# Optimization experiments

Measured on AMD Instinct MI355X. Metric: run time of the kernel, lower is better.

The kernel has to match this reference:

```python
import jax, jax.numpy as jnp
import numpy as np

N, K, D = 32768, 8192, 64

def setup_inputs() -> dict:
    key = jax.random.key(0)
    kx, kc = jax.random.split(key)
    x = jax.random.normal(kx, (N, D), dtype=jnp.float32)
    codebook = jax.random.normal(kc, (K, D), dtype=jnp.float32)
    return {"x": x, "codebook": codebook}

def reference(x, codebook):
    # Faithful to: argmin(((codebook[None] - x[:, None])**2).sum(-1), -1)
    # Computed via the expanded squared distance to avoid the [N, K, D]
    # constant per row and does not affect argmin, but we include it so the
    # distance matrix matches the original math exactly.
    x_sq = jnp.sum(x * x, axis=-1, keepdims=True)          # [N, 1]
    c_sq = jnp.sum(codebook * codebook, axis=-1)           # [K]
    cross = jnp.einsum('nd,kd->nk', x, codebook)           # [N, K]
    dists = x_sq - 2.0 * cross + c_sq[None, :]             # [N, K]
    return jnp.argmin(dists, axis=-1)                      # [N] int32
```

## Files before the change

kernel.cpp:

```cpp
#include <hip/hip_runtime.h>
#include <math.h>


typedef __attribute__((ext_vector_type(8)))  _Float16 h8v;
typedef __attribute__((ext_vector_type(16))) float f16v;

constexpr int NROWS = 32768;
constexpr int KC    = 8192;
constexpr int DD    = 64;
constexpr int TPB   = 512;
constexpr int PTPB  = 256;
constexpr int BROWS = 128;
constexpr int BTILE = 128;
constexpr int NT    = KC / BTILE;
constexpr int TILE_HALFS = BTILE * DD * 2;
constexpr int BUF_HALFS  = TILE_HALFS + 256;

__device__ __forceinline__ void split2h(float v, _Float16& h1, _Float16& h2) {
  const float av = fabsf(v);
  _Float16 a = (_Float16)v;
  if (av < 6.1035156e-5f) a = (_Float16)0.f;
  h1 = a;
  h2 = (_Float16)((v - (float)a) * 4096.f);
}

__device__ __forceinline__ void gload_lds16(const void* g, void* l) {
  __builtin_amdgcn_global_load_lds(
      (const __attribute__((address_space(1))) void*)g,
      (__attribute__((address_space(3))) void*)l, 16, 0, 0);
}
__device__ __forceinline__ void gload_lds4(const void* g, void* l) {
  __builtin_amdgcn_global_load_lds(
      (const __attribute__((address_space(1))) void*)g,
      (__attribute__((address_space(3))) void*)l, 4, 0, 0);
}

__device__ __forceinline__ unsigned fkey(float f) {
  const unsigned u = __float_as_uint(f);
  return u ^ (((unsigned)((int)u >> 31)) | 0x80000000u);
}

__global__ void vq_pre_kernel(const float* __restrict__ cb,
                              _Float16* __restrict__ bSwz,
                              float* __restrict__ csq) {
  const int gidx = blockIdx.x * PTPB + threadIdx.x;
  const int code = gidx >> 2;
  const int kc4  = gidx & 3;
  const float* cp = cb + (size_t)code * DD + kc4 * 16;
  float v[16];
#pragma unroll
  for (int d = 0; d < 16; d += 4) {
    const float4 g = *(const float4*)(cp + d);
    v[d] = g.x; v[d + 1] = g.y; v[d + 2] = g.z; v[d + 3] = g.w;
  }
  float s = 0.f;
#pragma unroll
  for (int d = 0; d < 16; ++d) s = fmaf(v[d], v[d], s);
  s += __shfl_xor(s, 1, 64);
  s += __shfl_xor(s, 2, 64);
  if (kc4 == 0) csq[code] = s;
  _Float16 p1[16], p2[16];
#pragma unroll
  for (int d = 0; d < 16; ++d) split2h(v[d], p1[d], p2[d]);
  const int g = code >> 5, l = code & 31;
  _Float16* base = bSwz + (size_t)g * 4096;
#pragma unroll
  for (int p = 0; p < 2; ++p) {
    const _Float16* pl = p ? p2 : p1;
#pragma unroll
    for (int h = 0; h < 2; ++h) {
      h8v wv;
#pragma unroll
      for (int j = 0; j < 8; ++j) wv[j] = pl[h * 8 + j];
      *(h8v*)(base + (p * 4 + kc4) * 512 + (h * 32 + l) * 8) = wv;
    }
  }
}

__global__ __launch_bounds__(TPB, 2)
void vq_mfma_kernel(const float* __restrict__ x, const _Float16* __restrict__ bSwz,
                    const float* __restrict__ csq_g, int* __restrict__ out) {
  __shared__ alignas(16) _Float16 ldsBf[3 * BUF_HALFS];
  __shared__ alignas(16) unsigned long long ldsRed[BROWS][4];

  const int tid  = threadIdx.x;
  const int lane = tid & 63;
  const int w    = tid >> 6;
  const int cg   = w & 3;
  const int rh   = w >> 2;
  const int half = lane >> 5;
  const int col  = lane & 31;
  const int wcode = cg * 32 + col;
  const int blockRow = blockIdx.x * BROWS;

#pragma unroll
  for (int tt = 0; tt < 2; ++tt) {
    const _Float16* gs = bSwz + (size_t)tt * TILE_HALFS + w * 512 + lane * 8;
    _Float16* ld = ldsBf + tt * BUF_HALFS + w * 512;
#pragma unroll
    for (int seg = 0; seg < 4; ++seg)
      gload_lds16(gs + seg * 4096, ld + seg * 4096);
    if (w < 2)
      gload_lds4(csq_g + tt * BTILE + w * 64 + lane,
                 (float*)(ldsBf + tt * BUF_HALFS + TILE_HALFS) + w * 64);
  }

  _Float16* ldsA2 = ldsBf + 2 * BUF_HALFS;
  {
    const int row = tid >> 2, dseg = (tid & 3) * 16;
    const float* xp = x + (size_t)(blockRow + row) * DD + dseg;
    float v[16];
#pragma unroll
    for (int d = 0; d < 16; d += 4) {
      const float4 g = *(const float4*)(xp + d);
      v[d] = g.x; v[d + 1] = g.y; v[d + 2] = g.z; v[d + 3] = g.w;
    }
    _Float16 qa[16], qb[16];
#pragma unroll
    for (int e = 0; e < 16; ++e) split2h(v[e], qa[e], qb[e]);
#pragma unroll
    for (int h2 = 0; h2 < 2; ++h2) {
      h8v a, b;
#pragma unroll
      for (int j = 0; j < 8; ++j) { a[j] = qa[h2 * 8 + j]; b[j] = qb[h2 * 8 + j]; }
      const int slot = (tid & 3) * 2 + h2;
      *(h8v*)&ldsA2[((0 * BROWS + row) * 8 + (slot ^ (row & 7))) * 8] = a;
      *(h8v*)&ldsA2[((1 * BROWS + row) * 8 + (slot ^ (row & 7))) * 8] = b;
    }
  }
  asm volatile("s_waitcnt lgkmcnt(0)\n\ts_barrier" ::: "memory");

  h8v afr[2][2][4];
#pragma unroll
  for (int q = 0; q < 2; ++q)
#pragma unroll
    for (int p = 0; p < 2; ++p)
#pragma unroll
      for (int kc = 0; kc < 4; ++kc) {
        const int arow = rh * 64 + q * 32 + col;
        const int slot = kc * 2 + half;
        afr[q][p][kc] =
            *(const h8v*)&ldsA2[((p * BROWS + arow) * 8 + (slot ^ (arow & 7))) * 8];
      }
  asm volatile("s_waitcnt vmcnt(4) lgkmcnt(0)\n\ts_barrier" ::: "memory");

  float bestD[32];
  unsigned bestC[32];
#pragma unroll
  for (int i = 0; i < 32; ++i) { bestD[i] = INFINITY; bestC[i] = 0u; }

  const f16v Z = {0.f,0.f,0.f,0.f,0.f,0.f,0.f,0.f,0.f,0.f,0.f,0.f,0.f,0.f,0.f,0.f};

  int buf = 0, pf = 2;
  for (int t = 0; t < NT; ++t) {
    if (t < NT - 2) {
      const _Float16* gs = bSwz + (size_t)(t + 2) * TILE_HALFS + w * 512 + lane * 8;
      _Float16* ld = ldsBf + pf * BUF_HALFS + w * 512;
#pragma unroll
      for (int seg = 0; seg < 4; ++seg)
        gload_lds16(gs + seg * 4096, ld + seg * 4096);
      if (w < 2)
        gload_lds4(csq_g + (t + 2) * BTILE + w * 64 + lane,
                   (float*)(ldsBf + pf * BUF_HALFS + TILE_HALFS) + w * 64);
    }
    const _Float16* bp = ldsBf + buf * BUF_HALFS;
    const _Float16* rb = bp + cg * 4096 + lane * 8;
    h8v b0[4], b1[4];
#pragma unroll
    for (int kc = 0; kc < 4; ++kc) {
      b0[kc] = *(const h8v*)(rb + kc * 512);
      b1[kc] = *(const h8v*)(rb + (4 + kc) * 512);
    }
    const float cs = ((const float*)(bp + TILE_HALFS))[wcode];

    f16v A0 = Z, B0 = Z, A1 = Z, B1 = Z;
#pragma unroll
    for (int kc = 0; kc < 4; ++kc) {
      A0 = __builtin_amdgcn_mfma_f32_32x32x16_f16(afr[0][0][kc], b0[kc], A0, 0, 0, 0);
      A1 = __builtin_amdgcn_mfma_f32_32x32x16_f16(afr[1][0][kc], b0[kc], A1, 0, 0, 0);
      B0 = __builtin_amdgcn_mfma_f32_32x32x16_f16(afr[0][0][kc], b1[kc], B0, 0, 0, 0);
      B1 = __builtin_amdgcn_mfma_f32_32x32x16_f16(afr[1][0][kc], b1[kc], B1, 0, 0, 0);
    }
#pragma unroll
    for (int kc = 0; kc < 4; ++kc) {
      B0 = __builtin_amdgcn_mfma_f32_32x32x16_f16(afr[0][1][kc], b0[kc], B0, 0, 0, 0);
      B1 = __builtin_amdgcn_mfma_f32_32x32x16_f16(afr[1][1][kc], b0[kc], B1, 0, 0, 0);
    }

    const unsigned code = (unsigned)(t * BTILE) + wcode;
#pragma unroll
    for (int i = 0; i < 16; ++i) {
      const float d0 = fmaf(-2.f, fmaf(B0[i], 2.44140625e-4f, A0[i]), cs);
      if (d0 < bestD[i])      { bestD[i] = d0;      bestC[i] = code; }
      const float d1 = fmaf(-2.f, fmaf(B1[i], 2.44140625e-4f, A1[i]), cs);
      if (d1 < bestD[16 + i]) { bestD[16 + i] = d1; bestC[16 + i] = code; }
    }

    if (t < NT - 2)
      asm volatile("s_waitcnt vmcnt(4) lgkmcnt(0)\n\ts_barrier" ::: "memory");
    else if (t == NT - 2)
      asm volatile("s_waitcnt vmcnt(0) lgkmcnt(0)\n\ts_barrier" ::: "memory");
    buf = (buf == 2) ? 0 : buf + 1;
    pf  = (pf == 2) ? 0 : pf + 1;
  }

  unsigned long long key[32];
#pragma unroll
  for (int i = 0; i < 32; ++i)
    key[i] = ((unsigned long long)fkey(bestD[i]) << 32) | bestC[i];
#pragma unroll
  for (int i = 0; i < 32; ++i) {
#pragma unroll
    for (int m = 1; m < 32; m <<= 1) {
      const unsigned long long o = __shfl_xor(key[i], m, 64);
      if (o < key[i]) key[i] = o;
    }
  }
  if (col == 0) {
#pragma unroll
    for (int i = 0; i < 32; ++i) {
      const int ii = i & 15, q = i >> 4;
      const int row = rh * 64 + q * 32 + (ii & 3) + 8 * (ii >> 2) + 4 * half;
      ldsRed[row][cg] = key[i];
    }
  }
  __syncthreads();
  if (tid < BROWS) {
    unsigned long long a = ldsRed[tid][0];
    const unsigned long long b = ldsRed[tid][1];
    const unsigned long long c = ldsRed[tid][2];
    const unsigned long long d = ldsRed[tid][3];
    if (b < a) a = b;
    if (c < a) a = c;
    if (d < a) a = d;
    out[blockRow + tid] = (int)(unsigned)(a & 0xFFFFFFFFull);
  }
}

extern "C" void kernel_launch(void* const* d_in, const int* in_sizes, int n_in,
                              void* d_out, int out_size, void* d_ws, size_t ws_size,
                              hipStream_t stream) {
  const float* x  = (const float*)d_in[0];
  const float* cb = (const float*)d_in[1];
  int* out = (int*)d_out;

  _Float16* bSwz = (_Float16*)d_ws;
  float* csq_g = (float*)((char*)d_ws + (size_t)KC * DD * 2 * 2);

  vq_pre_kernel<<<dim3(KC * 4 / PTPB), dim3(PTPB), 0, stream>>>(cb, bSwz, csq_g);
  vq_mfma_kernel<<<dim3(NROWS / BROWS), dim3(TPB), 0, stream>>>(
      x, bSwz, csq_g, out);
}
```

Baseline: 180.9 us.

## Halve block to 64 rows, double-buffer B tiles, and defer argmin update

```diff
diff --git a/kernel.cpp b/kernel.cpp
--- a/kernel.cpp
+++ b/kernel.cpp
@@ -8,9 +8,9 @@
 constexpr int NROWS = 32768;
 constexpr int KC    = 8192;
 constexpr int DD    = 64;
-constexpr int TPB   = 512;
+constexpr int TPB   = 256;
 constexpr int PTPB  = 256;
-constexpr int BROWS = 128;
+constexpr int BROWS = 64;
 constexpr int BTILE = 128;
 constexpr int NT    = KC / BTILE;
 constexpr int TILE_HALFS = BTILE * DD * 2;
@@ -80,32 +80,31 @@
 __global__ __launch_bounds__(TPB, 2)
 void vq_mfma_kernel(const float* __restrict__ x, const _Float16* __restrict__ bSwz,
                     const float* __restrict__ csq_g, int* __restrict__ out) {
-  __shared__ alignas(16) _Float16 ldsBf[3 * BUF_HALFS];
+  __shared__ alignas(16) _Float16 ldsBf[2 * BUF_HALFS];
   __shared__ alignas(16) unsigned long long ldsRed[BROWS][4];
 
   const int tid  = threadIdx.x;
   const int lane = tid & 63;
   const int w    = tid >> 6;
-  const int cg   = w & 3;
-  const int rh   = w >> 2;
   const int half = lane >> 5;
   const int col  = lane & 31;
-  const int wcode = cg * 32 + col;
+  const int wcode = w * 32 + col;
   const int blockRow = blockIdx.x * BROWS;
 
-#pragma unroll
-  for (int tt = 0; tt < 2; ++tt) {
-    const _Float16* gs = bSwz + (size_t)tt * TILE_HALFS + w * 512 + lane * 8;
-    _Float16* ld = ldsBf + tt * BUF_HALFS + w * 512;
-#pragma unroll
-    for (int seg = 0; seg < 4; ++seg)
-      gload_lds16(gs + seg * 4096, ld + seg * 4096);
-    if (w < 2)
-      gload_lds4(csq_g + tt * BTILE + w * 64 + lane,
-                 (float*)(ldsBf + tt * BUF_HALFS + TILE_HALFS) + w * 64);
-  }
-
-  _Float16* ldsA2 = ldsBf + 2 * BUF_HALFS;
+  {
+    const _Float16* gs = bSwz + tid * 8;
+    _Float16* ld = ldsBf + tid * 8;
+#pragma unroll
+    for (int seg = 0; seg < 8; ++seg)
+      gload_lds16(gs + seg * 2048, ld + seg * 2048);
+    if (w == 0) {
+      float* cslot = (float*)(ldsBf + TILE_HALFS);
+      gload_lds4(csq_g + lane, cslot);
+      gload_lds4(csq_g + 64 + lane, cslot + 64);
+    }
+  }
+
+  _Float16* ldsA = ldsBf + BUF_HALFS;
   {
     const int row = tid >> 2, dseg = (tid & 3) * 16;
     const float* xp = x + (size_t)(blockRow + row) * DD + dseg;
@@ -124,8 +123,8 @@
 #pragma unroll
       for (int j = 0; j < 8; ++j) { a[j] = qa[h2 * 8 + j]; b[j] = qb[h2 * 8 + j]; }
       const int slot = (tid & 3) * 2 + h2;
-      *(h8v*)&ldsA2[((0 * BROWS + row) * 8 + (slot ^ (row & 7))) * 8] = a;
-      *(h8v*)&ldsA2[((1 * BROWS + row) * 8 + (slot ^ (row & 7))) * 8] = b;
+      *(h8v*)&ldsA[(0 * 64 + row) * 64 + (slot ^ (row & 7)) * 8] = a;
+      *(h8v*)&ldsA[(1 * 64 + row) * 64 + (slot ^ (row & 7)) * 8] = b;
     }
   }
   asm volatile("s_waitcnt lgkmcnt(0)\n\ts_barrier" ::: "memory");
@@ -137,34 +136,42 @@
     for (int p = 0; p < 2; ++p)
 #pragma unroll
       for (int kc = 0; kc < 4; ++kc) {
-        const int arow = rh * 64 + q * 32 + col;
+        const int arow = q * 32 + col;
         const int slot = kc * 2 + half;
         afr[q][p][kc] =
-            *(const h8v*)&ldsA2[((p * BROWS + arow) * 8 + (slot ^ (arow & 7))) * 8];
+            *(const h8v*)&ldsA[(p * 64 + arow) * 64 + ((slot ^ (arow & 7))) * 8];
       }
-  asm volatile("s_waitcnt vmcnt(4) lgkmcnt(0)\n\ts_barrier" ::: "memory");
+  asm volatile("s_waitcnt vmcnt(0) lgkmcnt(0)\n\ts_barrier" ::: "memory");
 
   float bestD[32];
   unsigned bestC[32];
-#pragma unroll
-  for (int i = 0; i < 32; ++i) { bestD[i] = INFINITY; bestC[i] = 0u; }
+  float foldP[32];
+#pragma unroll
+  for (int i = 0; i < 32; ++i) {
+    bestD[i] = INFINITY; bestC[i] = 0u; foldP[i] = -INFINITY;
+  }
+  float csP = 0.f;
+  unsigned codeP = 0u;
 
   const f16v Z = {0.f,0.f,0.f,0.f,0.f,0.f,0.f,0.f,0.f,0.f,0.f,0.f,0.f,0.f,0.f,0.f};
 
-  int buf = 0, pf = 2;
+#pragma unroll 2
   for (int t = 0; t < NT; ++t) {
-    if (t < NT - 2) {
-      const _Float16* gs = bSwz + (size_t)(t + 2) * TILE_HALFS + w * 512 + lane * 8;
-      _Float16* ld = ldsBf + pf * BUF_HALFS + w * 512;
-#pragma unroll
-      for (int seg = 0; seg < 4; ++seg)
-        gload_lds16(gs + seg * 4096, ld + seg * 4096);
-      if (w < 2)
-        gload_lds4(csq_g + (t + 2) * BTILE + w * 64 + lane,
-                   (float*)(ldsBf + pf * BUF_HALFS + TILE_HALFS) + w * 64);
-    }
+    const int buf = t & 1;
     const _Float16* bp = ldsBf + buf * BUF_HALFS;
-    const _Float16* rb = bp + cg * 4096 + lane * 8;
+    if (t + 1 < NT) {
+      const _Float16* gs = bSwz + (size_t)(t + 1) * TILE_HALFS + tid * 8;
+      _Float16* ld = ldsBf + (buf ^ 1) * BUF_HALFS + tid * 8;
+#pragma unroll
+      for (int seg = 0; seg < 8; ++seg)
+        gload_lds16(gs + seg * 2048, ld + seg * 2048);
+      if (w == 0) {
+        float* cslot = (float*)(ldsBf + (buf ^ 1) * BUF_HALFS + TILE_HALFS);
+        gload_lds4(csq_g + (t + 1) * BTILE + lane, cslot);
+        gload_lds4(csq_g + (t + 1) * BTILE + 64 + lane, cslot + 64);
+      }
+    }
+    const _Float16* rb = bp + w * 4096 + lane * 8;
     h8v b0[4], b1[4];
 #pragma unroll
     for (int kc = 0; kc < 4; ++kc) {
@@ -173,35 +180,41 @@
     }
     const float cs = ((const float*)(bp + TILE_HALFS))[wcode];
 
-    f16v A0 = Z, B0 = Z, A1 = Z, B1 = Z;
+    __builtin_amdgcn_s_setprio(1);
+    f16v A0 = Z, B0v = Z, A1 = Z, B1v = Z;
 #pragma unroll
     for (int kc = 0; kc < 4; ++kc) {
-      A0 = __builtin_amdgcn_mfma_f32_32x32x16_f16(afr[0][0][kc], b0[kc], A0, 0, 0, 0);
-      A1 = __builtin_amdgcn_mfma_f32_32x32x16_f16(afr[1][0][kc], b0[kc], A1, 0, 0, 0);
-      B0 = __builtin_amdgcn_mfma_f32_32x32x16_f16(afr[0][0][kc], b1[kc], B0, 0, 0, 0);
-      B1 = __builtin_amdgcn_mfma_f32_32x32x16_f16(afr[1][0][kc], b1[kc], B1, 0, 0, 0);
+      A0  = __builtin_amdgcn_mfma_f32_32x32x16_f16(afr[0][0][kc], b0[kc], A0,  0, 0, 0);
+      A1  = __builtin_amdgcn_mfma_f32_32x32x16_f16(afr[1][0][kc], b0[kc], A1,  0, 0, 0);
+      B0v = __builtin_amdgcn_mfma_f32_32x32x16_f16(afr[0][0][kc], b1[kc], B0v, 0, 0, 0);
+      B1v = __builtin_amdgcn_mfma_f32_32x32x16_f16(afr[1][0][kc], b1[kc], B1v, 0, 0, 0);
     }
 #pragma unroll
     for (int kc = 0; kc < 4; ++kc) {
-      B0 = __builtin_amdgcn_mfma_f32_32x32x16_f16(afr[0][1][kc], b0[kc], B0, 0, 0, 0);
-      B1 = __builtin_amdgcn_mfma_f32_32x32x16_f16(afr[1][1][kc], b0[kc], B1, 0, 0, 0);
-    }
-
-    const unsigned code = (unsigned)(t * BTILE) + wcode;
+      B0v = __builtin_amdgcn_mfma_f32_32x32x16_f16(afr[0][1][kc], b0[kc], B0v, 0, 0, 0);
+      B1v = __builtin_amdgcn_mfma_f32_32x32x16_f16(afr[1][1][kc], b0[kc], B1v, 0, 0, 0);
+    }
+    __builtin_amdgcn_s_setprio(0);
+
+#pragma unroll
+    for (int i = 0; i < 32; ++i) {
+      const float d_ = fmaf(-2.f, foldP[i], csP);
+      if (d_ < bestD[i]) { bestD[i] = d_; bestC[i] = codeP; }
+    }
 #pragma unroll
     for (int i = 0; i < 16; ++i) {
-      const float d0 = fmaf(-2.f, fmaf(B0[i], 2.44140625e-4f, A0[i]), cs);
-      if (d0 < bestD[i])      { bestD[i] = d0;      bestC[i] = code; }
-      const float d1 = fmaf(-2.f, fmaf(B1[i], 2.44140625e-4f, A1[i]), cs);
-      if (d1 < bestD[16 + i]) { bestD[16 + i] = d1; bestC[16 + i] = code; }
-    }
-
-    if (t < NT - 2)
-      asm volatile("s_waitcnt vmcnt(4) lgkmcnt(0)\n\ts_barrier" ::: "memory");
-    else if (t == NT - 2)
-      asm volatile("s_waitcnt vmcnt(0) lgkmcnt(0)\n\ts_barrier" ::: "memory");
-    buf = (buf == 2) ? 0 : buf + 1;
-    pf  = (pf == 2) ? 0 : pf + 1;
+      foldP[i]      = fmaf(B0v[i], 2.44140625e-4f, A0[i]);
+      foldP[16 + i] = fmaf(B1v[i], 2.44140625e-4f, A1[i]);
+    }
+    csP = cs;
+    codeP = (unsigned)(t * BTILE) + wcode;
+
+    asm volatile("s_waitcnt vmcnt(0) lgkmcnt(0)\n\ts_barrier" ::: "memory");
+  }
+#pragma unroll
+  for (int i = 0; i < 32; ++i) {
+    const float d_ = fmaf(-2.f, foldP[i], csP);
+    if (d_ < bestD[i]) { bestD[i] = d_; bestC[i] = codeP; }
   }
 
   unsigned long long key[32];
@@ -220,8 +233,8 @@
 #pragma unroll
     for (int i = 0; i < 32; ++i) {
       const int ii = i & 15, q = i >> 4;
-      const int row = rh * 64 + q * 32 + (ii & 3) + 8 * (ii >> 2) + 4 * half;
-      ldsRed[row][cg] = key[i];
+      const int row = q * 32 + (ii & 3) + 8 * (ii >> 2) + 4 * half;
+      ldsRed[row][w] = key[i];
     }
   }
   __syncthreads();
```

Result: no change. 177.6 us (-1.8%).
